# Kernel tuning notes

Hardware: AMD Instinct MI355X
Metric: run time of the kernel (lower is better)

The kernel has to match this reference:

```python
import jax, jax.numpy as jnp
import numpy as np
import itertools

B, S, D, G = 4, 2048, 1024, 4
NG, NC = D // G, 2 ** G  # 256 groups, 16 codewords


def setup_inputs() -> dict:
    key = jax.random.key(0)
    k1, k2 = jax.random.split(key)
    x = jax.random.normal(k1, (B, S, D), dtype=jnp.float32)
    # Gumbel(0,1) noise, fixed for reproducibility
    u = jax.random.uniform(k2, (B, S, NG, NC), dtype=jnp.float32,
                           minval=1e-6, maxval=1.0 - 1e-6)
    gumbel = -jnp.log(-jnp.log(u))
    # all vertices of the {-1,+1}^G hypercube
    codebook = jnp.asarray(list(itertools.product([-1.0, 1.0], repeat=G)),
                           dtype=jnp.float32)  # [NC, G]
    log_temp = jnp.log(jnp.asarray(1.0, dtype=jnp.float32))  # scalar param
    return {"x": x, "gumbel": gumbel, "codebook": codebook, "log_temp": log_temp}


def reference(x, gumbel, codebook, log_temp):
    b, s, d = x.shape
    nc, g = codebook.shape
    ng = d // g
    groups = x.reshape(b, s, ng, g)                                  # [B,S,NG,G]
    cb_norm_sq = jnp.sum(codebook * codebook, axis=1)                # [NC]
    z_norm_sq = jnp.sum(groups * groups, axis=-1, keepdims=True)     # [B,S,NG,1]
    cross = jnp.einsum('bsng,cg->bsnc', groups, codebook)            # [B,S,NG,NC]
    logits = -(z_norm_sq - 2.0 * cross + cb_norm_sq)                 # -dist^2
    tau = jnp.clip(jnp.exp(log_temp), 0.05, 5.0)
    # gumbel-softmax (soft, hard=False)
    weights = jax.nn.softmax((logits + gumbel) / tau, axis=-1)       # [B,S,NG,NC]
    quantized = jnp.einsum('bsnc,cg->bsng', weights, codebook)       # [B,S,NG,G]
    return quantized.reshape(b, s, d)
```

## Files before the change

kernel.cpp:

```cpp
#include <hip/hip_runtime.h>

constexpr int B_ = 4;
constexpr int S_ = 2048;
constexpr int D_ = 1024;
constexpr int G_ = 4;
constexpr int NG_ = D_ / G_;
constexpr int NC_ = 1 << G_;
constexpr int NGROUPS = B_ * S_ * NG_;

typedef float f32x4 __attribute__((ext_vector_type(4)));

__global__ __launch_bounds__(256, 8) void gumbel_quant_kernel(
    const float* __restrict__ x,
    const float* __restrict__ gumbel,
    const float* __restrict__ codebook,
    const float* __restrict__ log_temp,
    float* __restrict__ out)
{
    __shared__ f32x4 lds[256 * 5];

    const int t = threadIdx.x;
    const int block0 = blockIdx.x * 256;

    const f32x4* gf4 = reinterpret_cast<const f32x4*>(gumbel) + (size_t)block0 * 4;
#pragma unroll
    for (int k = 0; k < 4; ++k) {
        const int e = k * 256 + t;
        const f32x4 v = __builtin_nontemporal_load(&gf4[e]);
        lds[(e >> 2) * 5 + (e & 3)] = v;
    }

    const f32x4 xg = __builtin_nontemporal_load(
        reinterpret_cast<const f32x4*>(x) + block0 + t);

    float tau = __expf(log_temp[0]);
    tau = fminf(fmaxf(tau, 0.05f), 5.0f);
    const float it1 = 1.0f / tau;
    const float it2 = 2.0f * it1;

    float hi[4], lo[4];
    {
        const float a = xg.x + xg.y, b = xg.x - xg.y;
        hi[3] = a;  hi[2] = b;  hi[1] = -b;  hi[0] = -a;
        const float c2 = xg.z + xg.w, d = xg.z - xg.w;
        lo[3] = c2; lo[2] = d;  lo[1] = -d;  lo[0] = -c2;
    }

    __syncthreads();

    f32x4 gq[4];
#pragma unroll
    for (int c4 = 0; c4 < 4; ++c4)
        gq[c4] = lds[t * 5 + c4];

    float sum = 0.0f;
    float q0 = 0.0f, q1 = 0.0f, q2 = 0.0f, q3 = 0.0f;
#pragma unroll
    for (int c = 0; c < NC_; ++c) {
        const float gv    = gq[c >> 2][c & 3];
        const float cross = hi[c >> 2] + lo[c & 3];
        const float v     = fmaf(cross, it2, gv * it1);
        const float e     = __expf(v);
        sum += e;
        q0 = (c & 8) ? (q0 + e) : (q0 - e);
        q1 = (c & 4) ? (q1 + e) : (q1 - e);
        q2 = (c & 2) ? (q2 + e) : (q2 - e);
        q3 = (c & 1) ? (q3 + e) : (q3 - e);
    }
    const float inv_sum = 1.0f / sum;

    f32x4 o;
    o.x = q0 * inv_sum;
    o.y = q1 * inv_sum;
    o.z = q2 * inv_sum;
    o.w = q3 * inv_sum;
    __builtin_nontemporal_store(o, reinterpret_cast<f32x4*>(out) + block0 + t);
}

extern "C" void kernel_launch(void* const* d_in, const int* in_sizes, int n_in,
                              void* d_out, int out_size, void* d_ws, size_t ws_size,
                              hipStream_t stream) {
    const float* x        = (const float*)d_in[0];
    const float* gumbel   = (const float*)d_in[1];
    const float* codebook = (const float*)d_in[2];
    const float* log_temp = (const float*)d_in[3];
    float* out = (float*)d_out;

    constexpr int block = 256;
    constexpr int grid = NGROUPS / block;
    gumbel_quant_kernel<<<grid, block, 0, stream>>>(x, gumbel, codebook, log_temp, out);
}
```

Baseline: 210.7 us.

## Split each group across four lanes with DPP quad reductions instead of LDS transpose

Each group's 16 codewords are now handled by four lanes, each computing four exponentials from its own float4 of gumbel noise. The partial sums are combined with DPP quad-permute shuffles, so the LDS staging buffer and barrier are gone. Each lane writes one scalar output. This launches four times as many threads with less work each, raising parallelism and removing LDS traffic. The cost is that x is loaded redundantly by four lanes and output stores are 4-byte instead of 16-byte.

```diff
diff --git a/kernel.cpp b/kernel.cpp
--- a/kernel.cpp
+++ b/kernel.cpp
@@ -8,7 +8,18 @@
 constexpr int NC_ = 1 << G_;
 constexpr int NGROUPS = B_ * S_ * NG_;
 
+constexpr int GROUPS_PER_BLOCK = 64;
+constexpr int NBLOCKS = NGROUPS / GROUPS_PER_BLOCK;
+
 typedef float f32x4 __attribute__((ext_vector_type(4)));
+
+template <int CTRL>
+__device__ __forceinline__ float qperm(float v) {
+    return __builtin_bit_cast(float,
+        __builtin_amdgcn_mov_dpp(__builtin_bit_cast(int, v), CTRL, 0xF, 0xF, true));
+}
+constexpr int QP_XOR1 = 0xB1;
+constexpr int QP_XOR2 = 0x4E;
 
 __global__ __launch_bounds__(256, 8) void gumbel_quant_kernel(
     const float* __restrict__ x,
@@ -17,64 +28,51 @@
     const float* __restrict__ log_temp,
     float* __restrict__ out)
 {
-    __shared__ f32x4 lds[256 * 5];
+    const int t = threadIdx.x;
+    const int l = t & 3;
+    const int g = blockIdx.x * GROUPS_PER_BLOCK + (t >> 2);
 
-    const int t = threadIdx.x;
-    const int block0 = blockIdx.x * 256;
-
-    const f32x4* gf4 = reinterpret_cast<const f32x4*>(gumbel) + (size_t)block0 * 4;
-#pragma unroll
-    for (int k = 0; k < 4; ++k) {
-        const int e = k * 256 + t;
-        const f32x4 v = __builtin_nontemporal_load(&gf4[e]);
-        lds[(e >> 2) * 5 + (e & 3)] = v;
-    }
-
+    const f32x4 gv = __builtin_nontemporal_load(
+        reinterpret_cast<const f32x4*>(gumbel) + (size_t)blockIdx.x * 256 + t);
     const f32x4 xg = __builtin_nontemporal_load(
-        reinterpret_cast<const f32x4*>(x) + block0 + t);
+        reinterpret_cast<const f32x4*>(x) + g);
 
     float tau = __expf(log_temp[0]);
     tau = fminf(fmaxf(tau, 0.05f), 5.0f);
     const float it1 = 1.0f / tau;
     const float it2 = 2.0f * it1;
 
-    float hi[4], lo[4];
-    {
-        const float a = xg.x + xg.y, b = xg.x - xg.y;
-        hi[3] = a;  hi[2] = b;  hi[1] = -b;  hi[0] = -a;
-        const float c2 = xg.z + xg.w, d = xg.z - xg.w;
-        lo[3] = c2; lo[2] = d;  lo[1] = -d;  lo[0] = -c2;
-    }
+    const float a = xg.x + xg.y, b = xg.x - xg.y;
+    const float base = (((l ^ (l >> 1)) & 1) ? b : a);
+    const float hi = (l & 2) ? base : -base;
+    const float lo3 = xg.z + xg.w, lo2 = xg.z - xg.w;
 
-    __syncthreads();
+    const float e0 = __expf(fmaf(hi - lo3, it2, gv.x * it1));
+    const float e1 = __expf(fmaf(hi - lo2, it2, gv.y * it1));
+    const float e2 = __expf(fmaf(hi + lo2, it2, gv.z * it1));
+    const float e3 = __expf(fmaf(hi + lo3, it2, gv.w * it1));
 
-    f32x4 gq[4];
-#pragma unroll
-    for (int c4 = 0; c4 < 4; ++c4)
-        gq[c4] = lds[t * 5 + c4];
+    const float s  = (e0 + e1) + (e2 + e3);
+    const float p2 = (e2 + e3) - (e0 + e1);
+    const float p3 = (e1 + e3) - (e0 + e2);
 
-    float sum = 0.0f;
-    float q0 = 0.0f, q1 = 0.0f, q2 = 0.0f, q3 = 0.0f;
-#pragma unroll
-    for (int c = 0; c < NC_; ++c) {
-        const float gv    = gq[c >> 2][c & 3];
-        const float cross = hi[c >> 2] + lo[c & 3];
-        const float v     = fmaf(cross, it2, gv * it1);
-        const float e     = __expf(v);
-        sum += e;
-        q0 = (c & 8) ? (q0 + e) : (q0 - e);
-        q1 = (c & 4) ? (q1 + e) : (q1 - e);
-        q2 = (c & 2) ? (q2 + e) : (q2 - e);
-        q3 = (c & 1) ? (q3 + e) : (q3 - e);
-    }
-    const float inv_sum = 1.0f / sum;
+    const float sA  = qperm<QP_XOR1>(s);
+    const float S1  = s + sA;
+    const float Bv  = (l & 1) ? (s - sA) : (sA - s);
+    const float p2s = p2 + qperm<QP_XOR1>(p2);
+    const float p3s = p3 + qperm<QP_XOR1>(p3);
+    const float S1b = qperm<QP_XOR2>(S1);
+    const float S   = S1 + S1b;
+    const float P0  = (l & 2) ? (S1 - S1b) : (S1b - S1);
+    const float P1  = Bv + qperm<QP_XOR2>(Bv);
+    const float P2  = p2s + qperm<QP_XOR2>(p2s);
+    const float P3  = p3s + qperm<QP_XOR2>(p3s);
 
-    f32x4 o;
-    o.x = q0 * inv_sum;
-    o.y = q1 * inv_sum;
-    o.z = q2 * inv_sum;
-    o.w = q3 * inv_sum;
-    __builtin_nontemporal_store(o, reinterpret_cast<f32x4*>(out) + block0 + t);
+    const float num = (l & 2) ? ((l & 1) ? P3 : P2)
+                              : ((l & 1) ? P1 : P0);
+    const float o = num * (1.0f / S);
+
+    __builtin_nontemporal_store(o, out + (size_t)blockIdx.x * 256 + t);
 }
 
 extern "C" void kernel_launch(void* const* d_in, const int* in_sizes, int n_in,
@@ -87,6 +85,5 @@
     float* out = (float*)d_out;
 
     constexpr int block = 256;
-    constexpr int grid = NGROUPS / block;
-    gumbel_quant_kernel<<<grid, block, 0, stream>>>(x, gumbel, codebook, log_temp, out);
+    gumbel_quant_kernel<<<NBLOCKS, block, 0, stream>>>(x, gumbel, codebook, log_temp, out);
 }
```

After: 210.1 us, median of 2. About the same (-0.3%).
